# Optimization experiments

Measured on AMD Instinct MI355X. Metric: run time of the kernel, lower is better.

The kernel has to match this reference:

```python
import jax, jax.numpy as jnp
import numpy as np

N, E, D, H = 20000, 320000, 128, 256
NUM_FINE = 2


def _mlp(x, W1, b1, W2, b2):
    # Linear -> relu -> Linear -> relu (dropout rate 0.0 is identity)
    h = jax.nn.relu(x @ W1 + b1)
    return jax.nn.relu(h @ W2 + b2)


def setup_inputs() -> dict:
    key = jax.random.key(0)
    ks = jax.random.split(key, 12)

    def p(k, shape):
        fan_in = shape[0]
        return jax.random.normal(k, shape, jnp.float32) * (1.0 / fan_in) ** 0.5

    return {
        "nodes": jax.random.normal(ks[0], (N, D), jnp.float32),
        "edges": jax.random.normal(ks[1], (E, D), jnp.float32),
        "senders": jax.random.randint(ks[2], (E,), 0, N, jnp.int32),
        "receivers": jax.random.randint(ks[3], (E,), 0, N, jnp.int32),
        # embed node MLP: D -> H -> D
        "Wn1": p(ks[4], (D, H)), "bn1": jnp.zeros((H,), jnp.float32),
        "Wn2": p(ks[5], (H, D)), "bn2": jnp.zeros((D,), jnp.float32),
        # embed edge MLP: D -> H -> D
        "We1": p(ks[6], (D, H)), "be1": jnp.zeros((H,), jnp.float32),
        "We2": p(ks[7], (H, D)), "be2": jnp.zeros((D,), jnp.float32),
        # edge model MLP: 3D -> H -> D  (concat[src, dest, edge_attr])
        "Wed1": p(ks[8], (3 * D, H)), "bed1": jnp.zeros((H,), jnp.float32),
        "Wed2": p(ks[9], (H, D)), "bed2": jnp.zeros((D,), jnp.float32),
        # node model MLP: 2D -> H -> D  (concat[x, segment_sum(edge_attr)])
        "Wnd1": p(ks[10], (2 * D, H)), "bnd1": jnp.zeros((H,), jnp.float32),
        "Wnd2": p(ks[11], (H, D)), "bnd2": jnp.zeros((D,), jnp.float32),
    }


def reference(nodes, edges, senders, receivers,
              Wn1, bn1, Wn2, bn2, We1, be1, We2, be2,
              Wed1, bed1, Wed2, bed2, Wnd1, bnd1, Wnd2, bnd2):
    # Embed stage (EmbedMetaLayer)
    x = _mlp(nodes, Wn1, bn1, Wn2, bn2)   # (N, D)
    e = _mlp(edges, We1, be1, We2, be2)   # (E, D)

    pooled = []
    for _ in range(NUM_FINE):
        # EdgeModel: gather src/dest node feats, concat with edge feats, MLP
        edge_in = jnp.concatenate([x[senders], x[receivers], e], axis=-1)  # (E, 3D)
        e = _mlp(edge_in, Wed1, bed1, Wed2, bed2)                           # (E, D)
        # NodeModel: scatter-add edge feats to receiver nodes, concat, MLP
        agg = jax.ops.segment_sum(e, receivers, num_segments=N)            # (N, D)
        x = _mlp(jnp.concatenate([x, agg], axis=-1), Wnd1, bnd1, Wnd2, bnd2)  # (N, D)
        # global_add_pooling: vmap(jnp.sum) over nodes -> per-node feature sum (N,)
        pooled.append(jnp.sum(x, axis=-1))
    # concatenate along last axis of the 1-D pooled vectors -> (NUM_FINE * N,)
    return jnp.concatenate(pooled, axis=-1)
```

## Files before the change

### kernel.cpp

```cpp
#include <hip/hip_runtime.h>
#include <stdint.h>

#define N_NODES 20000
#define N_EDGES 320000

typedef __attribute__((ext_vector_type(8)))  __bf16        bf16x8;
typedef __attribute__((ext_vector_type(16))) float         f32x16;
typedef __attribute__((ext_vector_type(4)))  float         f32x4v;
typedef __attribute__((ext_vector_type(4)))  uint32_t      u32x4;
typedef __attribute__((ext_vector_type(8)))  unsigned short us8;
typedef __attribute__((ext_vector_type(2)))  unsigned short us2;

static __device__ __forceinline__ unsigned short cvt_bf16(float f) {
  uint32_t u = __builtin_bit_cast(uint32_t, f);
  u = (u + 0x7fffu + ((u >> 16) & 1u)) >> 16;
  return (unsigned short)u;
}
static __device__ __forceinline__ float cvt_f32(unsigned short h) {
  uint32_t u = ((uint32_t)h) << 16;
  return __builtin_bit_cast(float, u);
}

static __device__ __forceinline__ void gll16(const void* g, void* l) {
  __builtin_amdgcn_global_load_lds(
      (const __attribute__((address_space(1))) unsigned int*)g,
      (__attribute__((address_space(3))) unsigned int*)l, 16, 0, 0);
}

#define WAITV(n) do { \
  if ((n) == 0)      asm volatile("s_waitcnt vmcnt(0)" ::: "memory"); \
  else if ((n) == 4) asm volatile("s_waitcnt vmcnt(4)" ::: "memory"); \
  else if ((n) == 8) asm volatile("s_waitcnt vmcnt(8)" ::: "memory"); \
  else               asm volatile("s_waitcnt vmcnt(12)" ::: "memory"); \
} while (0)

__global__ void pack_w(const float* __restrict__ W, unsigned short* __restrict__ out,
                       int K, int Ncols) {
  int idx = blockIdx.x * 256 + threadIdx.x;
  int total = K * Ncols;
  if (idx >= total) return;
  int e    = idx & 7;
  int lane = (idx >> 3) & 63;
  int t    = idx >> 9;
  int ntiles = Ncols >> 5;
  int nt = t % ntiles;
  int ks = t / ntiles;
  int k = ks * 16 + (lane >> 5) * 8 + e;
  int c = nt * 32 + (lane & 31);
  out[idx] = cvt_bf16(W[(size_t)k * Ncols + c]);
}

__global__ void pack_w2(const float* __restrict__ W, unsigned short* __restrict__ out) {
  int idx = blockIdx.x * 256 + threadIdx.x;
  if (idx >= 32768) return;
  int e    = idx & 7;
  int lane = (idx >> 3) & 63;
  int t    = idx >> 9;
  int nt = t & 3, ks = t >> 2;
  int k = ks * 16 + ((lane >> 5) << 2) + (e & 3) + ((e >> 2) << 3);
  int c = nt * 32 + (lane & 31);
  out[idx] = cvt_bf16(W[(size_t)k * 128 + c]);
}

__global__ void hist_k(const int* __restrict__ recv, int* __restrict__ cnt, int n) {
  int i = blockIdx.x * 256 + threadIdx.x;
  if (i < n) atomicAdd(&cnt[recv[i]], 1);
}

__global__ void scan_k(const int* __restrict__ cnt, int* __restrict__ off,
                       int* __restrict__ cursor, int n) {
  __shared__ int part[1024];
  int t = threadIdx.x;
  int chunk = (n + 1023) / 1024;
  int base = t * chunk;
  int s = 0;
  for (int i = 0; i < chunk; ++i) { int idx = base + i; if (idx < n) s += cnt[idx]; }
  part[t] = s;
  __syncthreads();
  for (int d = 1; d < 1024; d <<= 1) {
    int v = (t >= d) ? part[t - d] : 0;
    __syncthreads();
    part[t] += v;
    __syncthreads();
  }
  int prefix = (t > 0) ? part[t - 1] : 0;
  for (int i = 0; i < chunk; ++i) {
    int idx = base + i;
    if (idx < n) { off[idx] = prefix; cursor[idx] = prefix; prefix += cnt[idx]; }
  }
  if (t == 1023) off[n] = part[1023];
}

__global__ void fill_k(const int* __restrict__ recv, int* __restrict__ cursor,
                       int* __restrict__ eid, int n) {
  int i = blockIdx.x * 256 + threadIdx.x;
  if (i < n) {
    int p = atomicAdd(&cursor[recv[i]], 1);
    eid[p] = i;
  }
}

__global__ void agg_k(const unsigned short* __restrict__ eb, const int* __restrict__ off,
                      const int* __restrict__ eid, unsigned short* __restrict__ aggb, int n) {
  int node = blockIdx.x * 4 + (threadIdx.x >> 6);
  if (node >= n) return;
  int lane = threadIdx.x & 63;
  float a0 = 0.f, a1 = 0.f;
  int s = off[node], t = off[node + 1];
  for (int q = s; q < t; ++q) {
    int ei = eid[q];
    us2 v = *(const us2*)(eb + (size_t)ei * 128 + lane * 2);
    a0 += cvt_f32(v[0]);
    a1 += cvt_f32(v[1]);
  }
  us2 r; r[0] = cvt_bf16(a0); r[1] = cvt_bf16(a1);
  *(us2*)(aggb + (size_t)node * 128 + lane * 2) = r;
}

template <int KIN, int MODE, int POOL>
__global__ __launch_bounds__(256, 2)
void mlp_kernel(const float* __restrict__ srcf,
                const unsigned short* __restrict__ xb,
                const unsigned short* __restrict__ ebuf,
                const unsigned short* __restrict__ aggb,
                const int* __restrict__ senders,
                const int* __restrict__ receivers,
                const unsigned short* __restrict__ P1,
                const float* __restrict__ b1,
                const unsigned short* __restrict__ P2,
                const float* __restrict__ b2,
                unsigned short* __restrict__ dst,
                float* __restrict__ pool_out,
                int nrows) {
  constexpr int NS1 = KIN / 32;
  constexpr int NP  = NS1 / 2;
  __shared__ __align__(16) unsigned char lds[65536];

  const int tid  = threadIdx.x;
  const int lane = tid & 63;
  const int wid  = tid >> 6;
  const int g    = lane >> 5;
  const int l31  = lane & 31;
  const int rowBlock = blockIdx.x << 7;

  const unsigned char* P1b = (const unsigned char*)P1;
  const unsigned char* P2b = (const unsigned char*)P2;

  int grow = rowBlock + wid * 32 + l31;
  if (grow >= nrows) grow = nrows - 1;

  const unsigned short *pS = nullptr, *pR = nullptr, *pE = nullptr;
  const unsigned short *pX = nullptr, *pAg = nullptr;
  const float* fb = nullptr;
  if constexpr (MODE == 0) {
    fb = srcf + (size_t)grow * KIN;
  } else if constexpr (MODE == 1) {
    pS = xb + (size_t)senders[grow] * 128;
    pR = xb + (size_t)receivers[grow] * 128;
    pE = ebuf + (size_t)grow * 128;
  } else {
    pX  = xb + (size_t)grow * 128;
    pAg = aggb + (size_t)grow * 128;
  }

  auto STG1 = [&](int s) {
    unsigned char* bW = lds + (s & 3) * 16384;
#pragma unroll
    for (int c = 0; c < 4; ++c)
      gll16(P1b + (size_t)s * 16384 + c * 4096 + tid * 16,
            bW + c * 4096 + wid * 1024);
  };
  auto STG2 = [&](int c) {
    unsigned char* bW = lds + ((c + NS1) & 3) * 16384;
#pragma unroll
    for (int q = 0; q < 4; ++q)
      gll16(P2b + (size_t)c * 16384 + q * 4096 + tid * 16,
            bW + q * 4096 + wid * 1024);
  };

  auto LROW = [&](int s, us8* o) {
    const int k0s = s * 32;
    const unsigned short* p;
    if constexpr (MODE == 1) {
      const int seg = k0s >> 7;
      p = (seg == 0) ? pS : (seg == 1) ? pR : pE;
    } else {
      p = (k0s >> 7) ? pAg : pX;
    }
    const int ko = k0s & 127;
    o[0] = *(const us8*)(p + ko + g * 8);
    o[1] = *(const us8*)(p + ko + 16 + g * 8);
  };
  auto LROWF = [&](int s, f32x4v* rf) {
    const float* p = fb + s * 32 + g * 8;
    rf[0] = *(const f32x4v*)(p);
    rf[1] = *(const f32x4v*)(p + 4);
    rf[2] = *(const f32x4v*)(p + 16);
    rf[3] = *(const f32x4v*)(p + 20);
  };
  auto MKBR = [&](const f32x4v* rf, bf16x8& b0v, bf16x8& b1v) {
    us8 h0, h1;
#pragma unroll
    for (int e = 0; e < 4; ++e) {
      h0[e] = cvt_bf16(rf[0][e]); h0[4 + e] = cvt_bf16(rf[1][e]);
      h1[e] = cvt_bf16(rf[2][e]); h1[4 + e] = cvt_bf16(rf[3][e]);
    }
    b0v = __builtin_bit_cast(bf16x8, h0);
    b1v = __builtin_bit_cast(bf16x8, h1);
  };

  f32x16 acc1[8];
#pragma unroll
  for (int t = 0; t < 8; ++t)
#pragma unroll
    for (int k = 0; k < 16; ++k) acc1[t][k] = 0.0f;

  auto COMPUTE = [&](const unsigned char* bW, bf16x8 b0v, bf16x8 b1v) {
#pragma unroll
    for (int kc = 0; kc < 2; ++kc) {
      const bf16x8 bv = kc ? b1v : b0v;
#pragma unroll
      for (int nt = 0; nt < 8; ++nt) {
        bf16x8 av = __builtin_bit_cast(bf16x8,
            *(const us8*)(bW + (kc * 8 + nt) * 1024 + lane * 16));
        acc1[nt] = __builtin_amdgcn_mfma_f32_32x32x16_bf16(av, bv, acc1[nt], 0, 0, 0);
      }
    }
  };

  us8    rr[4][2];
  f32x4v rf[4][4];

  STG1(0); STG1(1);
  if constexpr (MODE == 0) { LROWF(0, rf[0]); LROWF(1, rf[1]); LROWF(2, rf[2]); LROWF(3, rf[3]); }
  else                     { LROW(0, rr[0]);  LROW(1, rr[1]);  LROW(2, rr[2]);  LROW(3, rr[3]); }

#pragma unroll
  for (int p = 0; p < NP; ++p) {
    const int s0 = 2 * p, s1 = 2 * p + 1;
    const int w = (p + 1 < NP) ? ((MODE == 0) ? 8 : 4) : 0;
    WAITV(w);
    asm volatile("s_waitcnt lgkmcnt(0)" ::: "memory");
    asm volatile("s_barrier" ::: "memory");

    bf16x8 a0v, a1v, c0v, c1v;
    if constexpr (MODE == 0) { MKBR(rf[s0 & 3], a0v, a1v); MKBR(rf[s1 & 3], c0v, c1v); }
    else {
      a0v = __builtin_bit_cast(bf16x8, rr[s0 & 3][0]); a1v = __builtin_bit_cast(bf16x8, rr[s0 & 3][1]);
      c0v = __builtin_bit_cast(bf16x8, rr[s1 & 3][0]); c1v = __builtin_bit_cast(bf16x8, rr[s1 & 3][1]);
    }

    if (p + 1 < NP) {
      STG1(s0 + 2); STG1(s1 + 2);
      if (p + 2 < NP) {
        if constexpr (MODE == 0) { LROWF(s0 + 4, rf[(s0 + 4) & 3]); LROWF(s1 + 4, rf[(s1 + 4) & 3]); }
        else                     { LROW(s0 + 4, rr[(s0 + 4) & 3]);  LROW(s1 + 4, rr[(s1 + 4) & 3]); }
      }
    }

    __builtin_amdgcn_s_setprio(1);
    COMPUTE(lds + (s0 & 3) * 16384, a0v, a1v);
    COMPUTE(lds + (s1 & 3) * 16384, c0v, c1v);
    __builtin_amdgcn_s_setprio(0);
  }

  STG2(0);
  STG2(1);

  u32x4 pa4[16];
#pragma unroll
  for (int t = 0; t < 8; ++t) {
#pragma unroll
    for (int q4 = 0; q4 < 4; ++q4) {
      const f32x4v bv4 = *(const f32x4v*)(b1 + t * 32 + q4 * 8 + g * 4);
      float v0 = fmaxf(acc1[t][q4 * 4 + 0] + bv4[0], 0.0f);
      float v1 = fmaxf(acc1[t][q4 * 4 + 1] + bv4[1], 0.0f);
      float v2 = fmaxf(acc1[t][q4 * 4 + 2] + bv4[2], 0.0f);
      float v3 = fmaxf(acc1[t][q4 * 4 + 3] + bv4[3], 0.0f);
      uint32_t lo, hi;
      asm("v_cvt_pk_bf16_f32 %0, %1, %2" : "=v"(lo) : "v"(v0), "v"(v1));
      asm("v_cvt_pk_bf16_f32 %0, %1, %2" : "=v"(hi) : "v"(v2), "v"(v3));
      pa4[t * 2 + (q4 >> 1)][(q4 & 1) * 2 + 0] = lo;
      pa4[t * 2 + (q4 >> 1)][(q4 & 1) * 2 + 1] = hi;
    }
  }

  f32x16 acc2[4];
#pragma unroll
  for (int nt = 0; nt < 4; ++nt)
#pragma unroll
    for (int k = 0; k < 16; ++k) acc2[nt][k] = 0.0f;

#pragma unroll
  for (int q = 0; q < 2; ++q) {
    WAITV(0);
    asm volatile("s_waitcnt lgkmcnt(0)" ::: "memory");
    asm volatile("s_barrier" ::: "memory");
    if (q == 0) { STG2(2); STG2(3); }
    __builtin_amdgcn_s_setprio(1);
#pragma unroll
    for (int ci = 0; ci < 2; ++ci) {
      const int c = q * 2 + ci;
      const unsigned char* bW = lds + ((c + NS1) & 3) * 16384;
#pragma unroll
      for (int kk = 0; kk < 4; ++kk) {
        const bf16x8 a2 = __builtin_bit_cast(bf16x8, pa4[c * 4 + kk]);
#pragma unroll
        for (int nt = 0; nt < 4; ++nt) {
          const bf16x8 bw = __builtin_bit_cast(bf16x8,
              *(const us8*)(bW + (kk * 4 + nt) * 1024 + lane * 16));
          acc2[nt] = __builtin_amdgcn_mfma_f32_32x32x16_bf16(a2, bw, acc2[nt], 0, 0, 0);
        }
      }
    }
    __builtin_amdgcn_s_setprio(0);
  }

  float bias2[4];
#pragma unroll
  for (int nt = 0; nt < 4; ++nt) bias2[nt] = b2[nt * 32 + l31];

#pragma unroll
  for (int reg = 0; reg < 16; ++reg) {
    const int rowpat = (reg & 3) + ((reg >> 2) << 3) + g * 4;
    const int row = rowBlock + wid * 32 + rowpat;
    float vs = 0.0f;
#pragma unroll
    for (int nt = 0; nt < 4; ++nt) {
      float v = fmaxf(acc2[nt][reg] + bias2[nt], 0.0f);
      vs += v;
      if (row < nrows) dst[(size_t)row * 128 + nt * 32 + l31] = cvt_bf16(v);
    }
    if constexpr (POOL) {
#pragma unroll
      for (int m = 1; m <= 16; m <<= 1) vs += __shfl_xor(vs, m, 64);
      if (l31 == 0 && row < nrows) pool_out[row] = vs;
    }
  }
}

static constexpr size_t OFF_X    = 0;
static constexpr size_t OFF_E    = 5120000;
static constexpr size_t OFF_AGG  = 87040000;
static constexpr size_t OFF_PN1  = 92160000;
static constexpr size_t OFF_PN2  = OFF_PN1 + 65536;
static constexpr size_t OFF_PE1  = OFF_PN2 + 65536;
static constexpr size_t OFF_PE2  = OFF_PE1 + 65536;
static constexpr size_t OFF_PD1  = OFF_PE2 + 65536;
static constexpr size_t OFF_PD2  = OFF_PD1 + 196608;
static constexpr size_t OFF_PM1  = OFF_PD2 + 65536;
static constexpr size_t OFF_PM2  = OFF_PM1 + 131072;
static constexpr size_t OFF_CNT  = OFF_PM2 + 65536;
static constexpr size_t OFF_OFFS = OFF_CNT + 80000;
static constexpr size_t OFF_CUR  = OFF_OFFS + 80004;
static constexpr size_t OFF_EID  = OFF_CUR + 80000;

extern "C" void kernel_launch(void* const* d_in, const int* in_sizes, int n_in,
                              void* d_out, int out_size, void* d_ws, size_t ws_size,
                              hipStream_t stream) {
  const float* nodes = (const float*)d_in[0];
  const float* edges = (const float*)d_in[1];
  const int* senders = (const int*)d_in[2];
  const int* receivers = (const int*)d_in[3];
  const float* Wn1 = (const float*)d_in[4];  const float* bn1 = (const float*)d_in[5];
  const float* Wn2 = (const float*)d_in[6];  const float* bn2 = (const float*)d_in[7];
  const float* We1 = (const float*)d_in[8];  const float* be1 = (const float*)d_in[9];
  const float* We2 = (const float*)d_in[10]; const float* be2 = (const float*)d_in[11];
  const float* Wed1 = (const float*)d_in[12]; const float* bed1 = (const float*)d_in[13];
  const float* Wed2 = (const float*)d_in[14]; const float* bed2 = (const float*)d_in[15];
  const float* Wnd1 = (const float*)d_in[16]; const float* bnd1 = (const float*)d_in[17];
  const float* Wnd2 = (const float*)d_in[18]; const float* bnd2 = (const float*)d_in[19];

  char* ws = (char*)d_ws;
  unsigned short* xb   = (unsigned short*)(ws + OFF_X);
  unsigned short* eb   = (unsigned short*)(ws + OFF_E);
  unsigned short* aggb = (unsigned short*)(ws + OFF_AGG);
  unsigned short* Pn1  = (unsigned short*)(ws + OFF_PN1);
  unsigned short* Pn2  = (unsigned short*)(ws + OFF_PN2);
  unsigned short* Pe1  = (unsigned short*)(ws + OFF_PE1);
  unsigned short* Pe2  = (unsigned short*)(ws + OFF_PE2);
  unsigned short* Pd1  = (unsigned short*)(ws + OFF_PD1);
  unsigned short* Pd2  = (unsigned short*)(ws + OFF_PD2);
  unsigned short* Pm1  = (unsigned short*)(ws + OFF_PM1);
  unsigned short* Pm2  = (unsigned short*)(ws + OFF_PM2);
  int* cnt    = (int*)(ws + OFF_CNT);
  int* offs   = (int*)(ws + OFF_OFFS);
  int* cursor = (int*)(ws + OFF_CUR);
  int* eid    = (int*)(ws + OFF_EID);
  float* outp = (float*)d_out;

  pack_w<<<128, 256, 0, stream>>>(Wn1, Pn1, 128, 256);
  pack_w2<<<128, 256, 0, stream>>>(Wn2, Pn2);
  pack_w<<<128, 256, 0, stream>>>(We1, Pe1, 128, 256);
  pack_w2<<<128, 256, 0, stream>>>(We2, Pe2);
  pack_w<<<384, 256, 0, stream>>>(Wed1, Pd1, 384, 256);
  pack_w2<<<128, 256, 0, stream>>>(Wed2, Pd2);
  pack_w<<<256, 256, 0, stream>>>(Wnd1, Pm1, 256, 256);
  pack_w2<<<128, 256, 0, stream>>>(Wnd2, Pm2);

  hipMemsetAsync(cnt, 0, (size_t)N_NODES * 4, stream);
  hist_k<<<1250, 256, 0, stream>>>(receivers, cnt, N_EDGES);
  scan_k<<<1, 1024, 0, stream>>>(cnt, offs, cursor, N_NODES);
  fill_k<<<1250, 256, 0, stream>>>(receivers, cursor, eid, N_EDGES);

  const int nodeBlocks = (N_NODES + 127) / 128;
  const int edgeBlocks = N_EDGES / 128;

  mlp_kernel<128, 0, 0><<<nodeBlocks, 256, 0, stream>>>(
      nodes, nullptr, nullptr, nullptr, nullptr, nullptr,
      Pn1, bn1, Pn2, bn2, xb, nullptr, N_NODES);
  mlp_kernel<128, 0, 0><<<edgeBlocks, 256, 0, stream>>>(
      edges, nullptr, nullptr, nullptr, nullptr, nullptr,
      Pe1, be1, Pe2, be2, eb, nullptr, N_EDGES);

  for (int it = 0; it < 2; ++it) {
    mlp_kernel<384, 1, 0><<<edgeBlocks, 256, 0, stream>>>(
        nullptr, xb, eb, nullptr, senders, receivers,
        Pd1, bed1, Pd2, bed2, eb, nullptr, N_EDGES);
    agg_k<<<(N_NODES + 3) / 4, 256, 0, stream>>>(eb, offs, eid, aggb, N_NODES);
    mlp_kernel<256, 2, 1><<<nodeBlocks, 256, 0, stream>>>(
        nullptr, xb, nullptr, aggb, nullptr, nullptr,
        Pm1, bnd1, Pm2, bnd2, xb, outp + (size_t)it * N_NODES, N_NODES);
  }
}
```

Before: 521.3 us.

## Store edge features in receiver-sorted order to make aggregation contiguous

Edge feature rows are now stored in receiver-sorted (CSR) order. The fill kernel records each edge's slot in that order, and the edge MLPs read and write edge rows through this permutation. The aggregation kernel can then stream each node's edges contiguously instead of gathering them through an edge-id indirection. In exchange, the edge MLP kernels now do indexed row reads and scattered row writes on the edge buffer.

Measured after the change: 497.7 us. 1.05x faster.

```diff
diff --git a/kernel.cpp b/kernel.cpp
--- a/kernel.cpp
+++ b/kernel.cpp
@@ -92,24 +92,23 @@
 }
 
 __global__ void fill_k(const int* __restrict__ recv, int* __restrict__ cursor,
-                       int* __restrict__ eid, int n) {
+                       int* __restrict__ pos, int n) {
   int i = blockIdx.x * 256 + threadIdx.x;
   if (i < n) {
     int p = atomicAdd(&cursor[recv[i]], 1);
-    eid[p] = i;
+    pos[i] = p;
   }
 }
 
 __global__ void agg_k(const unsigned short* __restrict__ eb, const int* __restrict__ off,
-                      const int* __restrict__ eid, unsigned short* __restrict__ aggb, int n) {
+                      unsigned short* __restrict__ aggb, int n) {
   int node = blockIdx.x * 4 + (threadIdx.x >> 6);
   if (node >= n) return;
   int lane = threadIdx.x & 63;
   float a0 = 0.f, a1 = 0.f;
   int s = off[node], t = off[node + 1];
   for (int q = s; q < t; ++q) {
-    int ei = eid[q];
-    us2 v = *(const us2*)(eb + (size_t)ei * 128 + lane * 2);
+    us2 v = *(const us2*)(eb + (size_t)q * 128 + lane * 2);
     a0 += cvt_f32(v[0]);
     a1 += cvt_f32(v[1]);
   }
@@ -125,6 +124,7 @@
                 const unsigned short* __restrict__ aggb,
                 const int* __restrict__ senders,
                 const int* __restrict__ receivers,
+                const int* __restrict__ perm,
                 const unsigned short* __restrict__ P1,
                 const float* __restrict__ b1,
                 const unsigned short* __restrict__ P2,
@@ -157,7 +157,7 @@
   } else if constexpr (MODE == 1) {
     pS = xb + (size_t)senders[grow] * 128;
     pR = xb + (size_t)receivers[grow] * 128;
-    pE = ebuf + (size_t)grow * 128;
+    pE = ebuf + (size_t)perm[grow] * 128;
   } else {
     pX  = xb + (size_t)grow * 128;
     pAg = aggb + (size_t)grow * 128;
@@ -324,17 +324,20 @@
   for (int reg = 0; reg < 16; ++reg) {
     const int rowpat = (reg & 3) + ((reg >> 2) << 3) + g * 4;
     const int row = rowBlock + wid * 32 + rowpat;
+    const bool ok = (row < nrows);
+    size_t drow = 0;
+    if (ok) drow = (size_t)((MODE <= 1 && perm) ? perm[row] : row);
     float vs = 0.0f;
 #pragma unroll
     for (int nt = 0; nt < 4; ++nt) {
       float v = fmaxf(acc2[nt][reg] + bias2[nt], 0.0f);
       vs += v;
-      if (row < nrows) dst[(size_t)row * 128 + nt * 32 + l31] = cvt_bf16(v);
+      if (ok) dst[drow * 128 + nt * 32 + l31] = cvt_bf16(v);
     }
     if constexpr (POOL) {
 #pragma unroll
       for (int m = 1; m <= 16; m <<= 1) vs += __shfl_xor(vs, m, 64);
-      if (l31 == 0 && row < nrows) pool_out[row] = vs;
+      if (l31 == 0 && ok) pool_out[row] = vs;
     }
   }
 }
@@ -353,7 +356,7 @@
 static constexpr size_t OFF_CNT  = OFF_PM2 + 65536;
 static constexpr size_t OFF_OFFS = OFF_CNT + 80000;
 static constexpr size_t OFF_CUR  = OFF_OFFS + 80004;
-static constexpr size_t OFF_EID  = OFF_CUR + 80000;
+static constexpr size_t OFF_POS  = OFF_CUR + 80000;
 
 extern "C" void kernel_launch(void* const* d_in, const int* in_sizes, int n_in,
                               void* d_out, int out_size, void* d_ws, size_t ws_size,
@@ -386,7 +389,7 @@
   int* cnt    = (int*)(ws + OFF_CNT);
   int* offs   = (int*)(ws + OFF_OFFS);
   int* cursor = (int*)(ws + OFF_CUR);
-  int* eid    = (int*)(ws + OFF_EID);
+  int* pos    = (int*)(ws + OFF_POS);
   float* outp = (float*)d_out;
 
   pack_w<<<128, 256, 0, stream>>>(Wn1, Pn1, 128, 256);
@@ -401,25 +404,25 @@
   hipMemsetAsync(cnt, 0, (size_t)N_NODES * 4, stream);
   hist_k<<<1250, 256, 0, stream>>>(receivers, cnt, N_EDGES);
   scan_k<<<1, 1024, 0, stream>>>(cnt, offs, cursor, N_NODES);
-  fill_k<<<1250, 256, 0, stream>>>(receivers, cursor, eid, N_EDGES);
+  fill_k<<<1250, 256, 0, stream>>>(receivers, cursor, pos, N_EDGES);
 
   const int nodeBlocks = (N_NODES + 127) / 128;
   const int edgeBlocks = N_EDGES / 128;
 
   mlp_kernel<128, 0, 0><<<nodeBlocks, 256, 0, stream>>>(
-      nodes, nullptr, nullptr, nullptr, nullptr, nullptr,
+      nodes, nullptr, nullptr, nullptr, nullptr, nullptr, nullptr,
       Pn1, bn1, Pn2, bn2, xb, nullptr, N_NODES);
   mlp_kernel<128, 0, 0><<<edgeBlocks, 256, 0, stream>>>(
-      edges, nullptr, nullptr, nullptr, nullptr, nullptr,
+      edges, nullptr, nullptr, nullptr, nullptr, nullptr, pos,
       Pe1, be1, Pe2, be2, eb, nullptr, N_EDGES);
 
   for (int it = 0; it < 2; ++it) {
     mlp_kernel<384, 1, 0><<<edgeBlocks, 256, 0, stream>>>(
-        nullptr, xb, eb, nullptr, senders, receivers,
+        nullptr, xb, eb, nullptr, senders, receivers, pos,
         Pd1, bed1, Pd2, bed2, eb, nullptr, N_EDGES);
-    agg_k<<<(N_NODES + 3) / 4, 256, 0, stream>>>(eb, offs, eid, aggb, N_NODES);
+    agg_k<<<(N_NODES + 3) / 4, 256, 0, stream>>>(eb, offs, aggb, N_NODES);
     mlp_kernel<256, 2, 1><<<nodeBlocks, 256, 0, stream>>>(
-        nullptr, xb, nullptr, aggb, nullptr, nullptr,
+        nullptr, xb, nullptr, aggb, nullptr, nullptr, nullptr,
         Pm1, bnd1, Pm2, bnd2, xb, outp + (size_t)it * N_NODES, N_NODES);
   }
 }
```
